# Optimization experiments

Hardware: AMD Instinct MI355X
Metric: run time of the kernel (lower is better)

The kernel has to match this reference:

```python
import jax, jax.numpy as jnp
import numpy as np

NUM_PERTS = 20000
D = 256          # embedding_dim
B, C = 64, 512   # batch_size, num_cells
EPS = 1e-5


def setup_inputs() -> dict:
    key = jax.random.key(0)
    ks = jax.random.split(key, 20)
    inp = {
        'perturbation_ids': jax.random.randint(ks[0], (B, C), 0, NUM_PERTS),
        'table': jax.random.normal(ks[1], (NUM_PERTS, D), dtype=jnp.float32),
    }
    s = 1.0 / np.sqrt(D)
    for i in range(4):
        inp[f'W{i+1}'] = jax.random.uniform(ks[2 + 2 * i], (D, D), minval=-s, maxval=s, dtype=jnp.float32)
        inp[f'b{i+1}'] = jax.random.uniform(ks[3 + 2 * i], (D,), minval=-s, maxval=s, dtype=jnp.float32)
    for i in range(3):
        inp[f'g{i+1}'] = jnp.ones((D,), jnp.float32)
        inp[f'be{i+1}'] = jnp.zeros((D,), jnp.float32)
    return inp


def _bn(x, gamma, beta):
    # BatchNorm1d forward with batch statistics (training-mode math, biased var)
    mu = jnp.mean(x, axis=0)
    var = jnp.mean(jnp.square(x - mu), axis=0)
    return (x - mu) * jax.lax.rsqrt(var + EPS) * gamma + beta


def reference(perturbation_ids, table,
              W1, b1, W2, b2, W3, b3, W4, b4,
              g1, be1, g2, be2, g3, be3):
    # Vectorized replacement of the Python double-loop dict gather
    emb = table[perturbation_ids]                 # (B, C, D)
    x = emb.reshape(-1, D)                        # (B*C, D)
    x = _bn(jax.nn.gelu(x @ W1 + b1, approximate=False), g1, be1)
    x = _bn(jax.nn.gelu(x @ W2 + b2, approximate=False), g2, be2)
    x = _bn(jax.nn.gelu(x @ W3 + b3, approximate=False), g3, be3)
    x = jax.nn.gelu(x @ W4 + b4, approximate=False)
    return x.reshape(B, C, D)
```

## Files before the change

### kernel.cpp

```cpp
#include <hip/hip_runtime.h>
#include <math.h>


typedef __attribute__((ext_vector_type(8))) short short8;
typedef __attribute__((ext_vector_type(4))) float floatx4;

#define DDIM 256
#define NBLK 512

struct Params {
    const int* ids;
    const float* table;
    const float* b[4];
    const float* g[3];
    const float* be[3];
    const unsigned short* Wt;
    float* stats;
    unsigned int* barrier;
    float* out;
};

__device__ __forceinline__ unsigned short f2bf(float f) {
    union { float f; unsigned int u; } v; v.f = f;
    unsigned int r = v.u + 0x7fffu + ((v.u >> 16) & 1u);
    return (unsigned short)(r >> 16);
}
__device__ __forceinline__ float bf2f(unsigned short u) {
    union { unsigned int i; float f; } v; v.i = ((unsigned int)u) << 16;
    return v.f;
}
__device__ __forceinline__ float gelu_fast(float x) {
    float z = 0.7978845608f * (x + 0.044715f * x * x * x);
    float e = __expf(2.0f * z);
    float th = 1.0f - 2.0f * __builtin_amdgcn_rcpf(1.0f + e);
    return 0.5f * x * (1.0f + th);
}

__global__ __launch_bounds__(256) void prep_kernel(
    const float* __restrict__ W0, const float* __restrict__ W1,
    const float* __restrict__ W2, const float* __restrict__ W3,
    unsigned short* __restrict__ Wt, float* __restrict__ stats,
    unsigned int* __restrict__ barrier)
{
    __shared__ unsigned short T[64][68];
    const int t = threadIdx.x, b = blockIdx.x;
    const int j  = b >> 4;
    const int kr = ((b >> 2) & 3) * 64;
    const int nc = (b & 3) * 64;
    const float* W = (j == 0) ? W0 : (j == 1) ? W1 : (j == 2) ? W2 : W3;

    {
        const int k = t >> 2, c0 = (t & 3) * 16;
        const float* src = W + (size_t)(kr + k) * DDIM + nc + c0;
#pragma unroll
        for (int i = 0; i < 4; ++i) {
            float4 v = *(const float4*)(src + i * 4);
            T[k][c0 + i * 4 + 0] = f2bf(v.x);
            T[k][c0 + i * 4 + 1] = f2bf(v.y);
            T[k][c0 + i * 4 + 2] = f2bf(v.z);
            T[k][c0 + i * 4 + 3] = f2bf(v.w);
        }
    }
    __syncthreads();
    {
        const int n = t >> 2, kc = (t & 3) * 16;
        union { unsigned short u[16]; uint4 v[2]; } o;
#pragma unroll
        for (int i = 0; i < 16; ++i) o.u[i] = T[kc + i][n];
        uint4* dst = (uint4*)(Wt + ((size_t)j << 16)
                              + (size_t)(nc + n) * DDIM + kr + kc);
        dst[0] = o.v[0]; dst[1] = o.v[1];
    }
    if (b < 48)       stats[b * 256 + t] = 0.f;
    else if (b < 52)  barrier[(b - 48) * 256 + t] = 0u;
}

__device__ __forceinline__ void grid_barrier(unsigned int* base, int phase)
{
    unsigned int* ph = base + phase * 256;
    __syncthreads();
    if (threadIdx.x == 0) {
        asm volatile("s_waitcnt vmcnt(0)" ::: "memory");
        unsigned int* gc   = ph + (blockIdx.x >> 6) * 16;
        unsigned int* root = ph + 128;
        unsigned int* flag = ph + 192;
        bool done = false;
        unsigned int old = __hip_atomic_fetch_add(gc, 1u, __ATOMIC_RELAXED,
                                                  __HIP_MEMORY_SCOPE_AGENT);
        if (old == 63u) {
            unsigned int r = __hip_atomic_fetch_add(root, 1u, __ATOMIC_RELAXED,
                                                    __HIP_MEMORY_SCOPE_AGENT);
            if (r == 7u) {
                __hip_atomic_store(flag, 1u, __ATOMIC_RELAXED,
                                   __HIP_MEMORY_SCOPE_AGENT);
                done = true;
            }
        }
        if (!done) {
            int cap = 2000000;
            while (!__hip_atomic_load(flag, __ATOMIC_RELAXED,
                                      __HIP_MEMORY_SCOPE_AGENT)) {
                __builtin_amdgcn_s_sleep(8);
                if (--cap == 0) break;
            }
        }
    }
    __syncthreads();
}

template<int GATHER, int LAST>
__device__ __forceinline__ void layer_step(
    unsigned short* P, float* sc, float* sh,
    const Params& p, floatx4 (&acc)[4][2],
    const unsigned short* Wt, const float* bias,
    const float* statsIn, const float* gma, const float* bta,
    float* statShards)
{
    const int tid  = threadIdx.x;
    const int blk  = blockIdx.x;
    const int wave = tid >> 6;
    const int lane = tid & 63;
    const int quad = lane >> 4;
    const int l15  = lane & 15;
    const int row0 = blk * 64;

    if (GATHER) {
        const int r     = tid >> 3;
        const int gbase = (tid & 7) * 4;
        const int src = p.ids[row0 + r];
        const float* tp = p.table + (size_t)src * DDIM + gbase * 8;
#pragma unroll
        for (int j = 0; j < 4; ++j) {
            float4 v0 = *(const float4*)(tp + j * 8);
            float4 v1 = *(const float4*)(tp + j * 8 + 4);
            union { unsigned short u[8]; uint4 v; } o;
            o.u[0]=f2bf(v0.x); o.u[1]=f2bf(v0.y); o.u[2]=f2bf(v0.z); o.u[3]=f2bf(v0.w);
            o.u[4]=f2bf(v1.x); o.u[5]=f2bf(v1.y); o.u[6]=f2bf(v1.z); o.u[7]=f2bf(v1.w);
            const int g = gbase + j;
            *(uint4*)(P + r * 256 + ((g ^ (r & 7)) << 3)) = o.v;
        }
    } else {
        if (tid < 256) {
            float sum = 0.f, sq = 0.f;
#pragma unroll
            for (int s = 0; s < 8; ++s) {
                sum += __hip_atomic_load(&statsIn[s * 512 + tid],
                                         __ATOMIC_RELAXED, __HIP_MEMORY_SCOPE_AGENT);
                sq  += __hip_atomic_load(&statsIn[s * 512 + 256 + tid],
                                         __ATOMIC_RELAXED, __HIP_MEMORY_SCOPE_AGENT);
            }
            const float mu  = sum * (1.f / 32768.f);
            const float var = sq * (1.f / 32768.f) - mu * mu;
            const float scl = rsqrtf(var + 1e-5f) * gma[tid];
            sc[tid] = scl;
            sh[tid] = bta[tid] - mu * scl;
        }
        __syncthreads();

#pragma unroll
        for (int mt = 0; mt < 4; ++mt) {
#pragma unroll
            for (int nt = 0; nt < 2; ++nt) {
                const int col = wave * 32 + nt * 16 + l15;
                const float scl = sc[col], shf = sh[col];
                const int gq = col >> 3, c7 = col & 7;
#pragma unroll
                for (int i = 0; i < 4; ++i) {
                    const int r = mt * 16 + quad * 4 + i;
                    const float a = fmaf(acc[mt][nt][i], scl, shf);
                    P[r * 256 + ((gq ^ (r & 7)) << 3) + c7] = f2bf(a);
                }
            }
        }
    }

    float bias_v[2];
#pragma unroll
    for (int nt = 0; nt < 2; ++nt)
        bias_v[nt] = bias[wave * 32 + nt * 16 + l15];

    __syncthreads();

#pragma unroll
    for (int i = 0; i < 4; ++i)
#pragma unroll
        for (int j = 0; j < 2; ++j)
            acc[i][j] = floatx4{0.f, 0.f, 0.f, 0.f};

    const unsigned short* wb = Wt + (size_t)(wave * 32 + l15) * DDIM + quad * 8;
    short8 bfr[2], bnx[2], af[4], anx[4];
    {
        const int agp = (quad ^ (l15 & 7)) * 8;
#pragma unroll
        for (int nt = 0; nt < 2; ++nt)
            bfr[nt] = *(const short8*)(wb + (size_t)(nt * 16) * DDIM);
#pragma unroll
        for (int mt = 0; mt < 4; ++mt)
            af[mt] = *(const short8*)(P + (mt * 16 + l15) * 256 + agp);
    }
#pragma unroll
    for (int kk = 0; kk < 8; ++kk) {
        if (kk < 7) {
            const int agp = (((kk + 1) * 4 + quad) ^ (l15 & 7)) * 8;
#pragma unroll
            for (int nt = 0; nt < 2; ++nt)
                bnx[nt] = *(const short8*)(wb + (size_t)(nt * 16) * DDIM
                                           + (kk + 1) * 32);
#pragma unroll
            for (int mt = 0; mt < 4; ++mt)
                anx[mt] = *(const short8*)(P + (mt * 16 + l15) * 256 + agp);
        }
#pragma unroll
        for (int mt = 0; mt < 4; ++mt)
#pragma unroll
            for (int nt = 0; nt < 2; ++nt)
                acc[mt][nt] = __builtin_amdgcn_mfma_f32_16x16x32_bf16(
                    af[mt], bfr[nt], acc[mt][nt], 0, 0, 0);
#pragma unroll
        for (int x = 0; x < 4; ++x) af[x] = anx[x];
#pragma unroll
        for (int x = 0; x < 2; ++x) bfr[x] = bnx[x];
    }

    if (LAST) {
#pragma unroll
        for (int mt = 0; mt < 4; ++mt)
#pragma unroll
            for (int nt = 0; nt < 2; ++nt) {
                const int col = wave * 32 + nt * 16 + l15;
#pragma unroll
                for (int i = 0; i < 4; ++i) {
                    const int r = mt * 16 + quad * 4 + i;
                    p.out[(size_t)(row0 + r) * DDIM + col] =
                        gelu_fast(acc[mt][nt][i] + bias_v[nt]);
                }
            }
    } else {
        float s1[2] = {0.f, 0.f};
        float s2[2] = {0.f, 0.f};
#pragma unroll
        for (int mt = 0; mt < 4; ++mt)
#pragma unroll
            for (int nt = 0; nt < 2; ++nt)
#pragma unroll
                for (int i = 0; i < 4; ++i) {
                    const float y = gelu_fast(acc[mt][nt][i] + bias_v[nt]);
                    acc[mt][nt][i] = y;
                    s1[nt] += y; s2[nt] += y * y;
                }
#pragma unroll
        for (int nt = 0; nt < 2; ++nt) {
            s1[nt] += __shfl_xor(s1[nt], 16); s1[nt] += __shfl_xor(s1[nt], 32);
            s2[nt] += __shfl_xor(s2[nt], 16); s2[nt] += __shfl_xor(s2[nt], 32);
        }
        float* sb = statShards + (blk & 7) * 512;
        if (quad == 0) {
#pragma unroll
            for (int nt = 0; nt < 2; ++nt) {
                const int col = wave * 32 + nt * 16 + l15;
                atomicAdd(&sb[col],       s1[nt]);
                atomicAdd(&sb[256 + col], s2[nt]);
            }
        }
    }
}

__global__ __launch_bounds__(512, 4) void fused_enc(Params p)
{
    __shared__ alignas(16) unsigned short P[64 * 256];
    __shared__ float sc[256], sh[256];

    floatx4 acc[4][2];

    layer_step<1, 0>(P, sc, sh, p, acc, p.Wt,          p.b[0],
                     nullptr,         nullptr, nullptr, p.stats);
    grid_barrier(p.barrier, 0);
    layer_step<0, 0>(P, sc, sh, p, acc, p.Wt + 65536,  p.b[1],
                     p.stats,         p.g[0],  p.be[0], p.stats + 4096);
    grid_barrier(p.barrier, 1);
    layer_step<0, 0>(P, sc, sh, p, acc, p.Wt + 131072, p.b[2],
                     p.stats + 4096,  p.g[1],  p.be[1], p.stats + 8192);
    grid_barrier(p.barrier, 2);
    layer_step<0, 1>(P, sc, sh, p, acc, p.Wt + 196608, p.b[3],
                     p.stats + 8192,  p.g[2],  p.be[2], nullptr);
}

extern "C" void kernel_launch(void* const* d_in, const int* in_sizes, int n_in,
                              void* d_out, int out_size, void* d_ws, size_t ws_size,
                              hipStream_t stream)
{
    const float* W1 = (const float*)d_in[2];
    const float* W2 = (const float*)d_in[4];
    const float* W3 = (const float*)d_in[6];
    const float* W4 = (const float*)d_in[8];

    Params pp;
    pp.ids   = (const int*)  d_in[0];
    pp.table = (const float*)d_in[1];
    pp.b[0] = (const float*)d_in[3];
    pp.b[1] = (const float*)d_in[5];
    pp.b[2] = (const float*)d_in[7];
    pp.b[3] = (const float*)d_in[9];
    pp.g[0] = (const float*)d_in[10]; pp.be[0] = (const float*)d_in[11];
    pp.g[1] = (const float*)d_in[12]; pp.be[1] = (const float*)d_in[13];
    pp.g[2] = (const float*)d_in[14]; pp.be[2] = (const float*)d_in[15];

    unsigned char* ws = (unsigned char*)d_ws;
    unsigned short* Wt = (unsigned short*)ws;
    float* stats       = (float*)(ws + (size_t)524288);
    unsigned int* bar  = (unsigned int*)(ws + (size_t)589824);

    pp.Wt      = Wt;
    pp.stats   = stats;
    pp.barrier = bar;
    pp.out     = (float*)d_out;

    prep_kernel<<<64, 256, 0, stream>>>(W1, W2, W3, W4, Wt, stats, bar);
    fused_enc<<<dim3(NBLK), dim3(512), 0, stream>>>(pp);
}
```

Before: 160.1 us.

## Retile waves to 2x4 MFMA layout and spread grid barrier release flags

Changes each wave's tile from 64 rows x 32 columns (4x2 MFMA tiles) to 32 rows x 64 columns (2x4). Each wave now loads fewer A fragments from LDS and more B fragments of W from global/L2, and stats atomics are spread across the eight shards by wave row. The grid barrier now gives each group of 64 blocks its own release flag, written by the last arriver, so spinning blocks poll different cache lines instead of one. The trade-off is more global weight traffic per wave and more atomics per stats column, in exchange for less LDS read traffic and less contention during the barrier spin.

```diff
diff --git a/kernel.cpp b/kernel.cpp
--- a/kernel.cpp
+++ b/kernel.cpp
@@ -72,18 +72,19 @@
         dst[0] = o.v[0]; dst[1] = o.v[1];
     }
     if (b < 48)       stats[b * 256 + t] = 0.f;
-    else if (b < 52)  barrier[(b - 48) * 256 + t] = 0u;
+    else if (b < 56)  barrier[(b - 48) * 256 + t] = 0u;
 }
 
 __device__ __forceinline__ void grid_barrier(unsigned int* base, int phase)
 {
-    unsigned int* ph = base + phase * 256;
+    unsigned int* ph = base + phase * 512;
     __syncthreads();
     if (threadIdx.x == 0) {
         asm volatile("s_waitcnt vmcnt(0)" ::: "memory");
-        unsigned int* gc   = ph + (blockIdx.x >> 6) * 16;
-        unsigned int* root = ph + 128;
-        unsigned int* flag = ph + 192;
+        const int g = blockIdx.x >> 6;
+        unsigned int* gc    = ph + g * 16;
+        unsigned int* root  = ph + 128;
+        unsigned int* gflag = ph + 256 + g * 16;
         bool done = false;
         unsigned int old = __hip_atomic_fetch_add(gc, 1u, __ATOMIC_RELAXED,
                                                   __HIP_MEMORY_SCOPE_AGENT);
@@ -91,14 +92,16 @@
             unsigned int r = __hip_atomic_fetch_add(root, 1u, __ATOMIC_RELAXED,
                                                     __HIP_MEMORY_SCOPE_AGENT);
             if (r == 7u) {
-                __hip_atomic_store(flag, 1u, __ATOMIC_RELAXED,
-                                   __HIP_MEMORY_SCOPE_AGENT);
+#pragma unroll
+                for (int i = 0; i < 8; ++i)
+                    __hip_atomic_store(ph + 256 + i * 16, 1u,
+                                       __ATOMIC_RELAXED, __HIP_MEMORY_SCOPE_AGENT);
                 done = true;
             }
         }
         if (!done) {
             int cap = 2000000;
-            while (!__hip_atomic_load(flag, __ATOMIC_RELAXED,
+            while (!__hip_atomic_load(gflag, __ATOMIC_RELAXED,
                                       __HIP_MEMORY_SCOPE_AGENT)) {
                 __builtin_amdgcn_s_sleep(8);
                 if (--cap == 0) break;
@@ -111,7 +114,7 @@
 template<int GATHER, int LAST>
 __device__ __forceinline__ void layer_step(
     unsigned short* P, float* sc, float* sh,
-    const Params& p, floatx4 (&acc)[4][2],
+    const Params& p, floatx4 (&acc)[2][4],
     const unsigned short* Wt, const float* bias,
     const float* statsIn, const float* gma, const float* bta,
     float* statShards)
@@ -119,6 +122,8 @@
     const int tid  = threadIdx.x;
     const int blk  = blockIdx.x;
     const int wave = tid >> 6;
+    const int wr   = wave & 1;
+    const int wc   = wave >> 1;
     const int lane = tid & 63;
     const int quad = lane >> 4;
     const int l15  = lane & 15;
@@ -158,15 +163,15 @@
         __syncthreads();
 
 #pragma unroll
-        for (int mt = 0; mt < 4; ++mt) {
-#pragma unroll
-            for (int nt = 0; nt < 2; ++nt) {
-                const int col = wave * 32 + nt * 16 + l15;
+        for (int mt = 0; mt < 2; ++mt) {
+#pragma unroll
+            for (int nt = 0; nt < 4; ++nt) {
+                const int col = wc * 64 + nt * 16 + l15;
                 const float scl = sc[col], shf = sh[col];
                 const int gq = col >> 3, c7 = col & 7;
 #pragma unroll
                 for (int i = 0; i < 4; ++i) {
-                    const int r = mt * 16 + quad * 4 + i;
+                    const int r = wr * 32 + mt * 16 + quad * 4 + i;
                     const float a = fmaf(acc[mt][nt][i], scl, shf);
                     P[r * 256 + ((gq ^ (r & 7)) << 3) + c7] = f2bf(a);
                 }
@@ -174,74 +179,74 @@
         }
     }
 
-    float bias_v[2];
-#pragma unroll
-    for (int nt = 0; nt < 2; ++nt)
-        bias_v[nt] = bias[wave * 32 + nt * 16 + l15];
+    float bias_v[4];
+#pragma unroll
+    for (int nt = 0; nt < 4; ++nt)
+        bias_v[nt] = bias[wc * 64 + nt * 16 + l15];
 
     __syncthreads();
 
 #pragma unroll
-    for (int i = 0; i < 4; ++i)
-#pragma unroll
-        for (int j = 0; j < 2; ++j)
+    for (int i = 0; i < 2; ++i)
+#pragma unroll
+        for (int j = 0; j < 4; ++j)
             acc[i][j] = floatx4{0.f, 0.f, 0.f, 0.f};
 
-    const unsigned short* wb = Wt + (size_t)(wave * 32 + l15) * DDIM + quad * 8;
-    short8 bfr[2], bnx[2], af[4], anx[4];
+    const unsigned short* wb = Wt + (size_t)(wc * 64 + l15) * DDIM + quad * 8;
+    short8 bfr[4], bnx[4], af[2], anx[2];
     {
         const int agp = (quad ^ (l15 & 7)) * 8;
 #pragma unroll
-        for (int nt = 0; nt < 2; ++nt)
+        for (int nt = 0; nt < 4; ++nt)
             bfr[nt] = *(const short8*)(wb + (size_t)(nt * 16) * DDIM);
 #pragma unroll
-        for (int mt = 0; mt < 4; ++mt)
-            af[mt] = *(const short8*)(P + (mt * 16 + l15) * 256 + agp);
+        for (int mt = 0; mt < 2; ++mt)
+            af[mt] = *(const short8*)(P + (wr * 32 + mt * 16 + l15) * 256 + agp);
     }
 #pragma unroll
     for (int kk = 0; kk < 8; ++kk) {
         if (kk < 7) {
             const int agp = (((kk + 1) * 4 + quad) ^ (l15 & 7)) * 8;
 #pragma unroll
-            for (int nt = 0; nt < 2; ++nt)
+            for (int nt = 0; nt < 4; ++nt)
                 bnx[nt] = *(const short8*)(wb + (size_t)(nt * 16) * DDIM
                                            + (kk + 1) * 32);
 #pragma unroll
-            for (int mt = 0; mt < 4; ++mt)
-                anx[mt] = *(const short8*)(P + (mt * 16 + l15) * 256 + agp);
-        }
-#pragma unroll
-        for (int mt = 0; mt < 4; ++mt)
-#pragma unroll
-            for (int nt = 0; nt < 2; ++nt)
+            for (int mt = 0; mt < 2; ++mt)
+                anx[mt] = *(const short8*)(P + (wr * 32 + mt * 16 + l15) * 256 + agp);
+        }
+#pragma unroll
+        for (int mt = 0; mt < 2; ++mt)
+#pragma unroll
+            for (int nt = 0; nt < 4; ++nt)
                 acc[mt][nt] = __builtin_amdgcn_mfma_f32_16x16x32_bf16(
                     af[mt], bfr[nt], acc[mt][nt], 0, 0, 0);
 #pragma unroll
-        for (int x = 0; x < 4; ++x) af[x] = anx[x];
-#pragma unroll
-        for (int x = 0; x < 2; ++x) bfr[x] = bnx[x];
+        for (int x = 0; x < 2; ++x) af[x] = anx[x];
+#pragma unroll
+        for (int x = 0; x < 4; ++x) bfr[x] = bnx[x];
     }
 
     if (LAST) {
 #pragma unroll
-        for (int mt = 0; mt < 4; ++mt)
-#pragma unroll
-            for (int nt = 0; nt < 2; ++nt) {
-                const int col = wave * 32 + nt * 16 + l15;
+        for (int mt = 0; mt < 2; ++mt)
+#pragma unroll
+            for (int nt = 0; nt < 4; ++nt) {
+                const int col = wc * 64 + nt * 16 + l15;
 #pragma unroll
                 for (int i = 0; i < 4; ++i) {
-                    const int r = mt * 16 + quad * 4 + i;
+                    const int r = wr * 32 + mt * 16 + quad * 4 + i;
                     p.out[(size_t)(row0 + r) * DDIM + col] =
                         gelu_fast(acc[mt][nt][i] + bias_v[nt]);
                 }
             }
     } else {
-        float s1[2] = {0.f, 0.f};
-        float s2[2] = {0.f, 0.f};
-#pragma unroll
-        for (int mt = 0; mt < 4; ++mt)
-#pragma unroll
-            for (int nt = 0; nt < 2; ++nt)
+        float s1[4] = {0.f, 0.f, 0.f, 0.f};
+        float s2[4] = {0.f, 0.f, 0.f, 0.f};
+#pragma unroll
+        for (int mt = 0; mt < 2; ++mt)
+#pragma unroll
+            for (int nt = 0; nt < 4; ++nt)
 #pragma unroll
                 for (int i = 0; i < 4; ++i) {
                     const float y = gelu_fast(acc[mt][nt][i] + bias_v[nt]);
@@ -249,15 +254,15 @@
                     s1[nt] += y; s2[nt] += y * y;
                 }
 #pragma unroll
-        for (int nt = 0; nt < 2; ++nt) {
+        for (int nt = 0; nt < 4; ++nt) {
             s1[nt] += __shfl_xor(s1[nt], 16); s1[nt] += __shfl_xor(s1[nt], 32);
             s2[nt] += __shfl_xor(s2[nt], 16); s2[nt] += __shfl_xor(s2[nt], 32);
         }
-        float* sb = statShards + (blk & 7) * 512;
+        float* sb = statShards + (((blk << 1) | wr) & 7) * 512;
         if (quad == 0) {
 #pragma unroll
-            for (int nt = 0; nt < 2; ++nt) {
-                const int col = wave * 32 + nt * 16 + l15;
+            for (int nt = 0; nt < 4; ++nt) {
+                const int col = wc * 64 + nt * 16 + l15;
                 atomicAdd(&sb[col],       s1[nt]);
                 atomicAdd(&sb[256 + col], s2[nt]);
             }
@@ -270,7 +275,7 @@
     __shared__ alignas(16) unsigned short P[64 * 256];
     __shared__ float sc[256], sh[256];
 
-    floatx4 acc[4][2];
+    floatx4 acc[2][4];
 
     layer_step<1, 0>(P, sc, sh, p, acc, p.Wt,          p.b[0],
                      nullptr,         nullptr, nullptr, p.stats);
```

New measurement: 188.4 us. 17.6% more time.

## Fold weight transpose/convert prep into fused kernel behind an extra grid barrier

Applied to the files above, without the earlier changes.

Removes the separate prep kernel. Each thread of the fused kernel now converts one weight element to bf16 in transposed layout and zeroes the stats, and layer 1 waits on a new grid barrier before its first MMA so that gather and bias loads overlap the prep. Barrier counters are cleared with a hipMemsetAsync instead. This trades a kernel launch and its serialization for a fourth grid-wide barrier, uncoalesced strided weight reads, and 2-byte atomic stores.

```diff
diff --git a/kernel.cpp b/kernel.cpp
--- a/kernel.cpp
+++ b/kernel.cpp
@@ -11,10 +11,11 @@
 struct Params {
     const int* ids;
     const float* table;
+    const float* W[4];
     const float* b[4];
     const float* g[3];
     const float* be[3];
-    const unsigned short* Wt;
+    unsigned short* Wt;
     float* stats;
     unsigned int* barrier;
     float* out;
@@ -34,45 +35,6 @@
     float e = __expf(2.0f * z);
     float th = 1.0f - 2.0f * __builtin_amdgcn_rcpf(1.0f + e);
     return 0.5f * x * (1.0f + th);
-}
-
-__global__ __launch_bounds__(256) void prep_kernel(
-    const float* __restrict__ W0, const float* __restrict__ W1,
-    const float* __restrict__ W2, const float* __restrict__ W3,
-    unsigned short* __restrict__ Wt, float* __restrict__ stats,
-    unsigned int* __restrict__ barrier)
-{
-    __shared__ unsigned short T[64][68];
-    const int t = threadIdx.x, b = blockIdx.x;
-    const int j  = b >> 4;
-    const int kr = ((b >> 2) & 3) * 64;
-    const int nc = (b & 3) * 64;
-    const float* W = (j == 0) ? W0 : (j == 1) ? W1 : (j == 2) ? W2 : W3;
-
-    {
-        const int k = t >> 2, c0 = (t & 3) * 16;
-        const float* src = W + (size_t)(kr + k) * DDIM + nc + c0;
-#pragma unroll
-        for (int i = 0; i < 4; ++i) {
-            float4 v = *(const float4*)(src + i * 4);
-            T[k][c0 + i * 4 + 0] = f2bf(v.x);
-            T[k][c0 + i * 4 + 1] = f2bf(v.y);
-            T[k][c0 + i * 4 + 2] = f2bf(v.z);
-            T[k][c0 + i * 4 + 3] = f2bf(v.w);
-        }
-    }
-    __syncthreads();
-    {
-        const int n = t >> 2, kc = (t & 3) * 16;
-        union { unsigned short u[16]; uint4 v[2]; } o;
-#pragma unroll
-        for (int i = 0; i < 16; ++i) o.u[i] = T[kc + i][n];
-        uint4* dst = (uint4*)(Wt + ((size_t)j << 16)
-                              + (size_t)(nc + n) * DDIM + kr + kc);
-        dst[0] = o.v[0]; dst[1] = o.v[1];
-    }
-    if (b < 48)       stats[b * 256 + t] = 0.f;
-    else if (b < 52)  barrier[(b - 48) * 256 + t] = 0u;
 }
 
 __device__ __forceinline__ void grid_barrier(unsigned int* base, int phase)
@@ -108,7 +70,7 @@
     __syncthreads();
 }
 
-template<int GATHER, int LAST>
+template<int GATHER, int LAST, int BAR0>
 __device__ __forceinline__ void layer_step(
     unsigned short* P, float* sc, float* sh,
     const Params& p, floatx4 (&acc)[4][2],
@@ -179,7 +141,8 @@
     for (int nt = 0; nt < 2; ++nt)
         bias_v[nt] = bias[wave * 32 + nt * 16 + l15];
 
-    __syncthreads();
+    if (BAR0) grid_barrier(p.barrier, 0);
+    else      __syncthreads();
 
 #pragma unroll
     for (int i = 0; i < 4; ++i)
@@ -270,51 +233,59 @@
     __shared__ alignas(16) unsigned short P[64 * 256];
     __shared__ float sc[256], sh[256];
 
+    const int tid = threadIdx.x, blk = blockIdx.x;
+
+    {
+        const int id  = blk * 512 + tid;
+        const int j   = id >> 16;
+        const int rem = id & 65535;
+        const int n   = rem >> 8;
+        const int k   = rem & 255;
+        const unsigned short w = f2bf(p.W[j][(size_t)k * DDIM + n]);
+        __hip_atomic_store(&p.Wt[((size_t)j << 16) + (size_t)n * DDIM + k], w,
+                           __ATOMIC_RELAXED, __HIP_MEMORY_SCOPE_AGENT);
+        if (blk < 48 && tid < 256)
+            __hip_atomic_store(&p.stats[blk * 256 + tid], 0.f,
+                               __ATOMIC_RELAXED, __HIP_MEMORY_SCOPE_AGENT);
+    }
+
     floatx4 acc[4][2];
 
-    layer_step<1, 0>(P, sc, sh, p, acc, p.Wt,          p.b[0],
-                     nullptr,         nullptr, nullptr, p.stats);
-    grid_barrier(p.barrier, 0);
-    layer_step<0, 0>(P, sc, sh, p, acc, p.Wt + 65536,  p.b[1],
-                     p.stats,         p.g[0],  p.be[0], p.stats + 4096);
+    layer_step<1, 0, 1>(P, sc, sh, p, acc, p.Wt,          p.b[0],
+                        nullptr,         nullptr, nullptr, p.stats);
     grid_barrier(p.barrier, 1);
-    layer_step<0, 0>(P, sc, sh, p, acc, p.Wt + 131072, p.b[2],
-                     p.stats + 4096,  p.g[1],  p.be[1], p.stats + 8192);
+    layer_step<0, 0, 0>(P, sc, sh, p, acc, p.Wt + 65536,  p.b[1],
+                        p.stats,         p.g[0],  p.be[0], p.stats + 4096);
     grid_barrier(p.barrier, 2);
-    layer_step<0, 1>(P, sc, sh, p, acc, p.Wt + 196608, p.b[3],
-                     p.stats + 8192,  p.g[2],  p.be[2], nullptr);
+    layer_step<0, 0, 0>(P, sc, sh, p, acc, p.Wt + 131072, p.b[2],
+                        p.stats + 4096,  p.g[1],  p.be[1], p.stats + 8192);
+    grid_barrier(p.barrier, 3);
+    layer_step<0, 1, 0>(P, sc, sh, p, acc, p.Wt + 196608, p.b[3],
+                        p.stats + 8192,  p.g[2],  p.be[2], nullptr);
 }
 
 extern "C" void kernel_launch(void* const* d_in, const int* in_sizes, int n_in,
                               void* d_out, int out_size, void* d_ws, size_t ws_size,
                               hipStream_t stream)
 {
-    const float* W1 = (const float*)d_in[2];
-    const float* W2 = (const float*)d_in[4];
-    const float* W3 = (const float*)d_in[6];
-    const float* W4 = (const float*)d_in[8];
-
     Params pp;
     pp.ids   = (const int*)  d_in[0];
     pp.table = (const float*)d_in[1];
-    pp.b[0] = (const float*)d_in[3];
-    pp.b[1] = (const float*)d_in[5];
-    pp.b[2] = (const float*)d_in[7];
-    pp.b[3] = (const float*)d_in[9];
+    pp.W[0] = (const float*)d_in[2];  pp.b[0] = (const float*)d_in[3];
+    pp.W[1] = (const float*)d_in[4];  pp.b[1] = (const float*)d_in[5];
+    pp.W[2] = (const float*)d_in[6];  pp.b[2] = (const float*)d_in[7];
+    pp.W[3] = (const float*)d_in[8];  pp.b[3] = (const float*)d_in[9];
     pp.g[0] = (const float*)d_in[10]; pp.be[0] = (const float*)d_in[11];
     pp.g[1] = (const float*)d_in[12]; pp.be[1] = (const float*)d_in[13];
     pp.g[2] = (const float*)d_in[14]; pp.be[2] = (const float*)d_in[15];
 
     unsigned char* ws = (unsigned char*)d_ws;
-    unsigned short* Wt = (unsigned short*)ws;
-    float* stats       = (float*)(ws + (size_t)524288);
-    unsigned int* bar  = (unsigned int*)(ws + (size_t)589824);
-
-    pp.Wt      = Wt;
-    pp.stats   = stats;
-    pp.barrier = bar;
+    pp.Wt      = (unsigned short*)ws;
+    pp.stats   = (float*)(ws + (size_t)524288);
+    pp.barrier = (unsigned int*)(ws + (size_t)589824);
     pp.out     = (float*)d_out;
 
-    prep_kernel<<<64, 256, 0, stream>>>(W1, W2, W3, W4, Wt, stats, bar);
+    hipMemsetAsync(ws + (size_t)589824, 0, 4096, stream);
+
     fused_enc<<<dim3(NBLK), dim3(512), 0, stream>>>(pp);
 }
```

New measurement: 168.1 us. +5.0%, slower.
